# Performance work log

Measured on AMD Instinct MI355X. Metric: run time of the kernel, lower is better.

Reference implementation:

```python
import jax, jax.numpy as jnp
import numpy as np

IN_F = 4096
OUT_F = 11008
GROUP = 128
GCOUNT = IN_F // GROUP      # 32
PACKS = IN_F // 8           # 512
TOKENS = 4096


def _pack_int4(nibbles):
    # nibbles: (..., K) int32 in [0,16) -> packed (..., K//8) int32
    shifts = jnp.arange(0, 32, 4, dtype=jnp.int32)
    r = nibbles.reshape(*nibbles.shape[:-1], nibbles.shape[-1] // 8, 8)
    return jnp.sum(r << shifts, axis=-1, dtype=jnp.int32)


def setup_inputs() -> dict:
    key = jax.random.key(0)
    k1, k2, k3, k4 = jax.random.split(key, 4)
    x = jax.random.normal(k1, (TOKENS, IN_F), dtype=jnp.float32)
    # generate int4 nibbles then pack along in_features (prepared AWQ layout: (O, K//8))
    nib = jax.random.randint(k2, (OUT_F, IN_F), 0, 16, dtype=jnp.int32)
    qweight = _pack_int4(nib)                              # (O, PACKS) int32
    qzeros = jax.random.randint(k3, (GCOUNT, OUT_F), 0, 16, dtype=jnp.int32)
    scales = (jax.random.uniform(k4, (GCOUNT, OUT_F), dtype=jnp.float32) * 0.02 + 0.001)
    return {"x": x, "qweight": qweight, "qzeros": qzeros, "scales": scales}


def _unpack_int4(packed):
    # packed: (O, K//8) int32 -> (O, K) int32 nibbles
    shifts = jnp.arange(0, 32, 4, dtype=jnp.int32)
    nib = (packed[:, :, None] >> shifts) & 15
    return nib.reshape(packed.shape[0], packed.shape[1] * 8)


def reference(x, qweight, qzeros, scales):
    # group-wise dequant: W[o,k] = (q[o,k] - zero[g,o]) * scale[g,o], g = k // GROUP
    nib = _unpack_int4(qweight).reshape(OUT_F, GCOUNT, GROUP)   # (O, Gc, G)
    z = qzeros.T[:, :, None].astype(jnp.float32)                # (O, Gc, 1)
    s = scales.T[:, :, None]                                    # (O, Gc, 1)
    W = ((nib.astype(jnp.float32) - z) * s).reshape(OUT_F, IN_F)
    # y = x @ W^T
    return jnp.einsum('tk,ok->to', x, W)
```

## Files before the change

### kernel.cpp

```cpp
#include <hip/hip_runtime.h>
#include <hip/hip_bf16.h>
#include <stdint.h>

#define TOKENS 4096
#define IN_F   4096
#define OUT_F  11008
#define PACKS  512
#define GCOUNT 32

#define BM 256
#define BN 256
#define BK 128
#define NKT (IN_F / BK)

typedef __attribute__((ext_vector_type(8))) short bf16x8;
typedef __attribute__((ext_vector_type(4))) float f32x4;
typedef __attribute__((ext_vector_type(4))) int i32x4;

#define AS1 __attribute__((address_space(1)))
#define AS3 __attribute__((address_space(3)))

static __device__ __forceinline__ short f2bf(float f) {
    union { __hip_bfloat16 h; short s; } u;
    u.h = __float2bfloat16(f);
    return u.s;
}

__global__ __launch_bounds__(256) void quant_x_kernel(const float* __restrict__ x,
                                                      signed char* __restrict__ xq,
                                                      float* __restrict__ sx) {
    const int row = blockIdx.x;
    const int t = threadIdx.x;
    const float4* src = (const float4*)(x + (size_t)row * IN_F);
    float4 v[4];
    float am = 0.0f;
#pragma unroll
    for (int i = 0; i < 4; ++i) {
        v[i] = src[t + 256 * i];
        am = fmaxf(am, fmaxf(fmaxf(fabsf(v[i].x), fabsf(v[i].y)),
                             fmaxf(fabsf(v[i].z), fabsf(v[i].w))));
    }
#pragma unroll
    for (int off = 32; off >= 1; off >>= 1)
        am = fmaxf(am, __shfl_xor(am, off));
    __shared__ float wmax[4];
    if ((t & 63) == 0) wmax[t >> 6] = am;
    __syncthreads();
    float amax = fmaxf(fmaxf(wmax[0], wmax[1]), fmaxf(wmax[2], wmax[3]));
    amax = fmaxf(amax, 1e-20f);
    const float rs = 127.0f / amax;
    int* dst = (int*)(xq + (size_t)row * IN_F);
#pragma unroll
    for (int i = 0; i < 4; ++i) {
        float fv[4] = {v[i].x, v[i].y, v[i].z, v[i].w};
        int p = 0;
#pragma unroll
        for (int j = 0; j < 4; ++j) {
            int q = __float2int_rn(fv[j] * rs);
            q = max(-127, min(127, q));
            p |= (q & 255) << (8 * j);
        }
        dst[t + 256 * i] = p;
    }
    if (t == 0) sx[row] = amax * (1.0f / 127.0f);
}

__global__ __launch_bounds__(256) void sw_kernel(const int* __restrict__ qz,
                                                 const float* __restrict__ sc,
                                                 float* __restrict__ sw,
                                                 float* __restrict__ rw) {
    int o = blockIdx.x * 256 + threadIdx.x;
    float wmax = 0.f;
#pragma unroll 8
    for (int g = 0; g < GCOUNT; ++g) {
        float s = sc[(size_t)g * OUT_F + o];
        int z = qz[(size_t)g * OUT_F + o];
        float m = (float)max(z, 15 - z);
        wmax = fmaxf(wmax, s * m);
    }
    sw[o] = wmax * (1.0f / 127.0f);
    rw[o] = 127.0f / wmax;
}

__global__ __launch_bounds__(256) void quant_w8_kernel(const int* __restrict__ qw,
                                                       const int* __restrict__ qz,
                                                       const float* __restrict__ sc,
                                                       const float* __restrict__ rw,
                                                       signed char* __restrict__ wq) {
    int i = blockIdx.x * 256 + threadIdx.x;
    int o = i >> 9, p = i & 511, g = p >> 4;
    int z = qz[(size_t)g * OUT_F + o];
    float f = sc[(size_t)g * OUT_F + o] * rw[o];
    int w = qw[i];
    int lo = 0, hi = 0;
#pragma unroll
    for (int j = 0; j < 4; ++j) {
        int d = __float2int_rn((float)(((w >> (4 * j)) & 15) - z) * f);
        d = max(-127, min(127, d));
        lo |= (d & 255) << (8 * j);
    }
#pragma unroll
    for (int j = 4; j < 8; ++j) {
        int d = __float2int_rn((float)(((w >> (4 * j)) & 15) - z) * f);
        d = max(-127, min(127, d));
        hi |= (d & 255) << (8 * (j - 4));
    }
    ((int2*)wq)[i] = make_int2(lo, hi);
}

__device__ __forceinline__ void stage_i8(const signed char* __restrict__ G, int grow0,
                                         int kt, signed char* lds, int tid) {
#pragma unroll
    for (int i = 0; i < 4; ++i) {
        int CH = i * 512 + tid;
        int r = CH >> 3;
        int c = (CH & 7) ^ (r & 7);
        const signed char* g = G + (size_t)(grow0 + r) * IN_F + kt + c * 16;
        __builtin_amdgcn_global_load_lds((const AS1 void*)g,
                                         (AS3 void*)(lds + CH * 16), 16, 0, 0);
    }
}

#define QUADI(AF, BF, AO, BO)                                                   \
    __builtin_amdgcn_s_setprio(1);                                              \
    _Pragma("unroll") for (int m = 0; m < 4; ++m)                               \
    _Pragma("unroll") for (int n = 0; n < 2; ++n)                               \
    _Pragma("unroll") for (int ks = 0; ks < 2; ++ks)                            \
        iacc[(AO) + m][(BO) + n] = __builtin_amdgcn_mfma_i32_16x16x64_i8(       \
            AF[m][ks], BF[n][ks], iacc[(AO) + m][(BO) + n], 0, 0, 0);           \
    __builtin_amdgcn_s_setprio(0);

__global__ __launch_bounds__(512, 2) void gemm_i8_kernel(const signed char* __restrict__ A,
                                                         const signed char* __restrict__ B,
                                                         const float* __restrict__ sw,
                                                         const float* __restrict__ sx,
                                                         float* __restrict__ C) {
    __shared__ signed char As[2][BM * BK];
    __shared__ signed char Bs[2][BN * BK];

    const int nbn = OUT_F / BN;
    const int nwg = (TOKENS / BM) * nbn;
    const int cpx = nwg >> 3;
    int bid = blockIdx.x;
    int swzb = (bid & 7) * cpx + (bid >> 3);
    int bm = swzb / nbn, bn = swzb % nbn;
    const int row0 = bm * BM, col0 = bn * BN;

    const int tid = threadIdx.x;
    const int lane = tid & 63;
    const int wid = tid >> 6;
    const int wm = wid >> 2, wn = wid & 3;
    const int l15 = lane & 15, lhi = lane >> 4, l7 = lane & 7;
    const int cs0 = ((lhi ^ l7) & 7) * 16;
    const int cs1 = (((4 + lhi) ^ l7) & 7) * 16;
    const int rdA = (wm * 128 + l15) * BK;
    const int rdB = (wn * 64 + l15) * BK;

    i32x4 iacc[8][4] = {};
    i32x4 afA[4][2], afB[4][2], bfA[2][2], bfB[2][2];

    stage_i8(A, row0, 0, &As[0][0], tid);
    stage_i8(B, col0, 0, &Bs[0][0], tid);
    stage_i8(A, row0, BK, &As[1][0], tid);
    asm volatile("s_waitcnt vmcnt(4)" ::: "memory");
    __builtin_amdgcn_s_barrier();

    for (int t = 0; t < NKT; ++t) {
        const int cab = t & 1;
        const signed char* At = &As[cab][0];
        const signed char* Bt = &Bs[cab][0];

#pragma unroll
        for (int m = 0; m < 4; ++m) {
            afA[m][0] = *(const i32x4*)(At + rdA + m * 2048 + cs0);
            afA[m][1] = *(const i32x4*)(At + rdA + m * 2048 + cs1);
        }
        if (t + 1 < NKT) stage_i8(B, col0, (t + 1) * BK, &Bs[cab ^ 1][0], tid);
        __builtin_amdgcn_sched_barrier(0);
        if (t > 0) { QUADI(afB, bfA, 4, 0); }

#pragma unroll
        for (int n = 0; n < 2; ++n) {
            bfA[n][0] = *(const i32x4*)(Bt + rdB + n * 2048 + cs0);
            bfA[n][1] = *(const i32x4*)(Bt + rdB + n * 2048 + cs1);
        }
        __builtin_amdgcn_sched_barrier(0);
        if (t > 0) { QUADI(afB, bfB, 4, 2); }

#pragma unroll
        for (int n = 0; n < 2; ++n) {
            bfB[n][0] = *(const i32x4*)(Bt + rdB + (2 + n) * 2048 + cs0);
            bfB[n][1] = *(const i32x4*)(Bt + rdB + (2 + n) * 2048 + cs1);
        }
#pragma unroll
        for (int m = 0; m < 4; ++m) {
            afB[m][0] = *(const i32x4*)(At + rdA + (4 + m) * 2048 + cs0);
            afB[m][1] = *(const i32x4*)(At + rdA + (4 + m) * 2048 + cs1);
        }
        __builtin_amdgcn_sched_barrier(0);
        QUADI(afA, bfA, 0, 0);
        asm volatile("s_waitcnt lgkmcnt(0)" ::: "memory");
        __builtin_amdgcn_sched_barrier(0);
        __builtin_amdgcn_s_barrier();

        if (t + 2 < NKT) stage_i8(A, row0, (t + 2) * BK, &As[cab][0], tid);
        __builtin_amdgcn_sched_barrier(0);
        QUADI(afA, bfB, 0, 2);
        if (t < NKT - 2) {
            asm volatile("s_waitcnt vmcnt(4)" ::: "memory");
        } else if (t == NKT - 2) {
            asm volatile("s_waitcnt vmcnt(0)" ::: "memory");
        }
        __builtin_amdgcn_s_barrier();
    }

    { QUADI(afB, bfA, 4, 0); }
    { QUADI(afB, bfB, 4, 2); }

#pragma unroll
    for (int m = 0; m < 8; ++m) {
        const int rbase = row0 + wm * 128 + m * 16 + lhi * 4;
        f32x4 s4 = *(const f32x4*)(sx + rbase);
#pragma unroll
        for (int n = 0; n < 4; ++n) {
            const int c = col0 + wn * 64 + n * 16 + l15;
            const float swc = sw[c];
#pragma unroll
            for (int j = 0; j < 4; ++j)
                C[(size_t)(rbase + j) * OUT_F + c] = s4[j] * swc * (float)iacc[m][n][j];
        }
    }
}

__device__ __forceinline__ void mfma_tile128(const short* As, const short* Bs,
                                             f32x4 acc[4][4], int lane, int wm, int wn) {
#pragma unroll
    for (int kk = 0; kk < 64; kk += 32) {
        const int kb = kk + (lane >> 4) * 8;
        bf16x8 af[4], bfr[4];
#pragma unroll
        for (int m = 0; m < 4; ++m) {
            int r = wm * 64 + m * 16 + (lane & 15);
            af[m] = *(const bf16x8*)(As + r * 64 + kb);
        }
#pragma unroll
        for (int n = 0; n < 4; ++n) {
            int c = wn * 64 + n * 16 + (lane & 15);
            bfr[n] = *(const bf16x8*)(Bs + c * 64 + kb);
        }
#pragma unroll
        for (int m = 0; m < 4; ++m)
#pragma unroll
            for (int n = 0; n < 4; ++n)
                acc[m][n] = __builtin_amdgcn_mfma_f32_16x16x32_bf16(af[m], bfr[n],
                                                                    acc[m][n], 0, 0, 0);
    }
}

__global__ __launch_bounds__(256) void gemm_fused_kernel(const float* __restrict__ x,
                                                         const int* __restrict__ qw,
                                                         const int* __restrict__ qz,
                                                         const float* __restrict__ sc,
                                                         float* __restrict__ C) {
    const int nbn = OUT_F / 128;
    const int nwg = (TOKENS / 128) * nbn;
    const int cpx = nwg >> 3;
    int bid = blockIdx.x;
    int swzb = (bid & 7) * cpx + (bid >> 3);
    int bm = swzb / nbn, bn = swzb % nbn;
    const int row0 = bm * 128, col0 = bn * 128;

    __shared__ short As[128 * 64];
    __shared__ short Bs[128 * 64];

    const int tid = threadIdx.x;
    const int lane = tid & 63;
    const int wid = tid >> 6;
    const int wm = wid >> 1, wn = wid & 1;

    f32x4 acc[4][4] = {};

    for (int kt = 0; kt < IN_F; kt += 64) {
#pragma unroll
        for (int i = 0; i < 4; ++i) {
            int idx = i * 256 + tid;
            int r = idx >> 3, kc = (idx & 7) * 8;
            const float4* src = (const float4*)(x + (size_t)(row0 + r) * IN_F + kt + kc);
            float4 a = src[0], b = src[1];
            bf16x8 v;
            v[0] = f2bf(a.x); v[1] = f2bf(a.y); v[2] = f2bf(a.z); v[3] = f2bf(a.w);
            v[4] = f2bf(b.x); v[5] = f2bf(b.y); v[6] = f2bf(b.z); v[7] = f2bf(b.w);
            *(bf16x8*)(As + r * 64 + kc) = v;
        }
        {
            int ol = tid >> 1;
            int kc = (tid & 1) * 32;
            const int4* src = (const int4*)(qw + (size_t)(col0 + ol) * PACKS + ((kt + kc) >> 3));
            int4 w4 = *src;
            int g = kt >> 7;
            float z = (float)qz[(size_t)g * OUT_F + col0 + ol];
            float s = sc[(size_t)g * OUT_F + col0 + ol];
            float zs = z * s;
            const int* wp = (const int*)&w4;
#pragma unroll
            for (int c2 = 0; c2 < 4; ++c2) {
                int w32 = wp[c2];
                bf16x8 v;
#pragma unroll
                for (int j = 0; j < 8; ++j)
                    v[j] = f2bf((float)((w32 >> (4 * j)) & 15) * s - zs);
                *(bf16x8*)(Bs + ol * 64 + kc + c2 * 8) = v;
            }
        }
        __syncthreads();
        mfma_tile128(As, Bs, acc, lane, wm, wn);
        __syncthreads();
    }
#pragma unroll
    for (int m = 0; m < 4; ++m)
#pragma unroll
        for (int n = 0; n < 4; ++n) {
            int r = row0 + wm * 64 + m * 16 + ((lane >> 4) << 2);
            int c = col0 + wn * 64 + n * 16 + (lane & 15);
#pragma unroll
            for (int j = 0; j < 4; ++j)
                C[(size_t)(r + j) * OUT_F + c] = acc[m][n][j];
        }
}

extern "C" void kernel_launch(void* const* d_in, const int* in_sizes, int n_in,
                              void* d_out, int out_size, void* d_ws, size_t ws_size,
                              hipStream_t stream) {
    const float* x = (const float*)d_in[0];
    const int* qw = (const int*)d_in[1];
    const int* qz = (const int*)d_in[2];
    const float* sc = (const float*)d_in[3];
    float* out = (float*)d_out;

    const size_t xq_b = (size_t)TOKENS * IN_F;
    const size_t sx_b = (size_t)TOKENS * 4;
    const size_t sw_b = (size_t)OUT_F * 4;
    const size_t wq_b = (size_t)OUT_F * IN_F;
    const size_t need = xq_b + sx_b + 2 * sw_b + wq_b;

    if (ws_size >= need) {
        signed char* xq = (signed char*)d_ws;
        float* sx = (float*)((char*)d_ws + xq_b);
        float* sw = (float*)((char*)d_ws + xq_b + sx_b);
        float* rw = (float*)((char*)d_ws + xq_b + sx_b + sw_b);
        signed char* wq = (signed char*)((char*)d_ws + xq_b + sx_b + 2 * sw_b);
        quant_x_kernel<<<TOKENS, 256, 0, stream>>>(x, xq, sx);
        sw_kernel<<<OUT_F / 256, 256, 0, stream>>>(qz, sc, sw, rw);
        quant_w8_kernel<<<(OUT_F * PACKS) / 256, 256, 0, stream>>>(qw, qz, sc, rw, wq);
        const int ngemm = (TOKENS / BM) * (OUT_F / BN);
        gemm_i8_kernel<<<ngemm, 512, 0, stream>>>(xq, wq, sw, sx, out);
    } else {
        gemm_fused_kernel<<<(TOKENS / 128) * (OUT_F / 128), 256, 0, stream>>>(x, qw, qz, sc, out);
    }
}
```

Before: 257.7 us.

## Switch int8 GEMM from 16x16x64 to 32x32x32 MFMA tiles

Replaces the 16x16x64 int8 MFMA with the 32x32x32 variant. Each wave's 128x64 tile is now covered by 4x2 larger blocks with 16-element accumulators, and the K dimension is split into four 32-wide sub-steps. LDS fragment reads, the swizzled column offsets and the epilogue row mapping are reworked to match the new output layout. This is meant to raise operand reuse per LDS read and cut the instruction count, but it reshuffles the software pipeline and may change register pressure.

New measurement: 270.0 us. 4.8% more time.

```diff
diff --git a/kernel.cpp b/kernel.cpp
--- a/kernel.cpp
+++ b/kernel.cpp
@@ -16,6 +16,7 @@
 typedef __attribute__((ext_vector_type(8))) short bf16x8;
 typedef __attribute__((ext_vector_type(4))) float f32x4;
 typedef __attribute__((ext_vector_type(4))) int i32x4;
+typedef __attribute__((ext_vector_type(16))) int i32x16;
 
 #define AS1 __attribute__((address_space(1)))
 #define AS3 __attribute__((address_space(3)))
@@ -121,13 +122,18 @@
     }
 }
 
-#define QUADI(AF, BF, AO, BO)                                                   \
+#define READK(S)                                                                \
+    _Pragma("unroll") for (int m = 0; m < 4; ++m)                               \
+        a[S][m] = *(const i32x4*)(At + rA[m] + csk[S]);                         \
+    _Pragma("unroll") for (int n = 0; n < 2; ++n)                               \
+        b[S][n] = *(const i32x4*)(Bt + rB[n] + csk[S]);
+
+#define OCTI(S)                                                                 \
     __builtin_amdgcn_s_setprio(1);                                              \
     _Pragma("unroll") for (int m = 0; m < 4; ++m)                               \
     _Pragma("unroll") for (int n = 0; n < 2; ++n)                               \
-    _Pragma("unroll") for (int ks = 0; ks < 2; ++ks)                            \
-        iacc[(AO) + m][(BO) + n] = __builtin_amdgcn_mfma_i32_16x16x64_i8(       \
-            AF[m][ks], BF[n][ks], iacc[(AO) + m][(BO) + n], 0, 0, 0);           \
+        acc[m][n] = __builtin_amdgcn_mfma_i32_32x32x32_i8(                      \
+            a[S][m], b[S][n], acc[m][n], 0, 0, 0);                              \
     __builtin_amdgcn_s_setprio(0);
 
 __global__ __launch_bounds__(512, 2) void gemm_i8_kernel(const signed char* __restrict__ A,
@@ -150,14 +156,20 @@
     const int lane = tid & 63;
     const int wid = tid >> 6;
     const int wm = wid >> 2, wn = wid & 3;
-    const int l15 = lane & 15, lhi = lane >> 4, l7 = lane & 7;
-    const int cs0 = ((lhi ^ l7) & 7) * 16;
-    const int cs1 = (((4 + lhi) ^ l7) & 7) * 16;
-    const int rdA = (wm * 128 + l15) * BK;
-    const int rdB = (wn * 64 + l15) * BK;
-
-    i32x4 iacc[8][4] = {};
-    i32x4 afA[4][2], afB[4][2], bfA[2][2], bfB[2][2];
+    const int l31 = lane & 31, lh5 = lane >> 5, l7 = lane & 7;
+
+    int csk[4];
+#pragma unroll
+    for (int s = 0; s < 4; ++s)
+        csk[s] = ((2 * s + lh5) ^ l7) * 16;
+    int rA[4], rB[2];
+#pragma unroll
+    for (int m = 0; m < 4; ++m) rA[m] = (wm * 128 + m * 32 + l31) * BK;
+#pragma unroll
+    for (int n = 0; n < 2; ++n) rB[n] = (wn * 64 + n * 32 + l31) * BK;
+
+    i32x16 acc[4][2] = {};
+    i32x4 a[4][4], b[4][2];
 
     stage_i8(A, row0, 0, &As[0][0], tid);
     stage_i8(B, col0, 0, &Bs[0][0], tid);
@@ -170,42 +182,26 @@
         const signed char* At = &As[cab][0];
         const signed char* Bt = &Bs[cab][0];
 
-#pragma unroll
-        for (int m = 0; m < 4; ++m) {
-            afA[m][0] = *(const i32x4*)(At + rdA + m * 2048 + cs0);
-            afA[m][1] = *(const i32x4*)(At + rdA + m * 2048 + cs1);
-        }
+        READK(0);
         if (t + 1 < NKT) stage_i8(B, col0, (t + 1) * BK, &Bs[cab ^ 1][0], tid);
         __builtin_amdgcn_sched_barrier(0);
-        if (t > 0) { QUADI(afB, bfA, 4, 0); }
-
-#pragma unroll
-        for (int n = 0; n < 2; ++n) {
-            bfA[n][0] = *(const i32x4*)(Bt + rdB + n * 2048 + cs0);
-            bfA[n][1] = *(const i32x4*)(Bt + rdB + n * 2048 + cs1);
-        }
-        __builtin_amdgcn_sched_barrier(0);
-        if (t > 0) { QUADI(afB, bfB, 4, 2); }
-
-#pragma unroll
-        for (int n = 0; n < 2; ++n) {
-            bfB[n][0] = *(const i32x4*)(Bt + rdB + (2 + n) * 2048 + cs0);
-            bfB[n][1] = *(const i32x4*)(Bt + rdB + (2 + n) * 2048 + cs1);
-        }
-#pragma unroll
-        for (int m = 0; m < 4; ++m) {
-            afB[m][0] = *(const i32x4*)(At + rdA + (4 + m) * 2048 + cs0);
-            afB[m][1] = *(const i32x4*)(At + rdA + (4 + m) * 2048 + cs1);
-        }
-        __builtin_amdgcn_sched_barrier(0);
-        QUADI(afA, bfA, 0, 0);
+        if (t > 0) { OCTI(2); }
+
+        READK(1);
+        __builtin_amdgcn_sched_barrier(0);
+        if (t > 0) { OCTI(3); }
+
+        READK(2);
+        READK(3);
+        __builtin_amdgcn_sched_barrier(0);
+        OCTI(0);
         asm volatile("s_waitcnt lgkmcnt(0)" ::: "memory");
         __builtin_amdgcn_sched_barrier(0);
         __builtin_amdgcn_s_barrier();
 
         if (t + 2 < NKT) stage_i8(A, row0, (t + 2) * BK, &As[cab][0], tid);
         __builtin_amdgcn_sched_barrier(0);
-        QUADI(afA, bfB, 0, 2);
+        OCTI(1);
         if (t < NKT - 2) {
             asm volatile("s_waitcnt vmcnt(4)" ::: "memory");
         } else if (t == NKT - 2) {
@@ -214,20 +210,26 @@
         __builtin_amdgcn_s_barrier();
     }
 
-    { QUADI(afB, bfA, 4, 0); }
-    { QUADI(afB, bfB, 4, 2); }
-
-#pragma unroll
-    for (int m = 0; m < 8; ++m) {
-        const int rbase = row0 + wm * 128 + m * 16 + lhi * 4;
-        f32x4 s4 = *(const f32x4*)(sx + rbase);
-#pragma unroll
-        for (int n = 0; n < 4; ++n) {
-            const int c = col0 + wn * 64 + n * 16 + l15;
+    { OCTI(2); }
+    { OCTI(3); }
+
+#pragma unroll
+    for (int m = 0; m < 4; ++m) {
+        const int rb = row0 + wm * 128 + m * 32 + 4 * lh5;
+        f32x4 sxv[4];
+#pragma unroll
+        for (int g = 0; g < 4; ++g)
+            sxv[g] = *(const f32x4*)(sx + rb + 8 * g);
+#pragma unroll
+        for (int n = 0; n < 2; ++n) {
+            const int c = col0 + wn * 64 + n * 32 + l31;
             const float swc = sw[c];
 #pragma unroll
-            for (int j = 0; j < 4; ++j)
-                C[(size_t)(rbase + j) * OUT_F + c] = s4[j] * swc * (float)iacc[m][n][j];
+            for (int j = 0; j < 16; ++j) {
+                const int g = j >> 2, jj = j & 3;
+                const int r = rb + 8 * g + jj;
+                C[(size_t)r * OUT_F + c] = sxv[g][jj] * swc * (float)acc[m][n][j];
+            }
         }
     }
 }
@@ -286,10 +288,10 @@
             int idx = i * 256 + tid;
             int r = idx >> 3, kc = (idx & 7) * 8;
             const float4* src = (const float4*)(x + (size_t)(row0 + r) * IN_F + kt + kc);
-            float4 a = src[0], b = src[1];
+            float4 aa = src[0], bb = src[1];
             bf16x8 v;
-            v[0] = f2bf(a.x); v[1] = f2bf(a.y); v[2] = f2bf(a.z); v[3] = f2bf(a.w);
-            v[4] = f2bf(b.x); v[5] = f2bf(b.y); v[6] = f2bf(b.z); v[7] = f2bf(b.w);
+            v[0] = f2bf(aa.x); v[1] = f2bf(aa.y); v[2] = f2bf(aa.z); v[3] = f2bf(aa.w);
+            v[4] = f2bf(bb.x); v[5] = f2bf(bb.y); v[6] = f2bf(bb.z); v[7] = f2bf(bb.w);
             *(bf16x8*)(As + r * 64 + kc) = v;
         }
         {
```
